# Kernel tuning notes

Hardware: AMD Instinct MI355X
Metric: run time of the kernel (lower is better)

Reference implementation:

```python
import jax, jax.numpy as jnp
import numpy as np

M, N, C = 384, 384, 16
DN = ('NCHW', 'OIHW', 'NCHW')

def _rconv(x, w):
    # real-valued 2D cross-correlation, padding=4 (9x9 kernel, SAME)
    return jax.lax.conv_general_dilated(x, w, (1, 1), ((4, 4), (4, 4)), dimension_numbers=DN)

def _cconv(x, w):
    # complex conv2d decomposed into 4 real convs (matches torch complex conv2d)
    xr, xi, wr, wi = x.real, x.imag, w.real, w.imag
    return (_rconv(xr, wr) - _rconv(xi, wi)) + 1j * (_rconv(xr, wi) + _rconv(xi, wr))

def setup_inputs() -> dict:
    key = jax.random.key(0)
    ks = jax.random.split(key, 8)
    shp = (1, M, N, 2 * C)
    kspace = jax.random.normal(ks[0], shp, jnp.float32)
    row_keep = (jax.random.uniform(ks[1], (M,)) < 0.45).astype(jnp.float32)
    kspace = kspace * row_keep[None, :, None, None]
    z = 0.1 * jax.random.normal(ks[2], shp, jnp.float32)
    prev_kspace = 0.1 * jax.random.normal(ks[3], shp, jnp.float32)
    kernel_r = 0.05 * jax.random.normal(ks[4], (1, 81, C, C), jnp.float32)
    kernel_i = 0.05 * jax.random.normal(ks[5], (1, 81, C, C), jnp.float32)
    miu = jnp.array([0.05], jnp.float32)
    spirit_kernels = jnp.zeros((1,), jnp.float32)  # unused by the module's math
    return {"z": z, "kspace": kspace, "kernel_r": kernel_r, "kernel_i": kernel_i,
            "spirit_kernels": spirit_kernels, "prev_kspace": prev_kspace, "miu": miu}

def _forward(z, kspace, kernel_r, kernel_i, prev_kspace, miu):
    divp = kspace.shape[3] // 2
    kk = kspace[0, :, :, :divp] + 1j * kspace[0, :, :, divp:]  # [m,n,C] complex64
    m, n, no_c = kk.shape
    locs = jnp.abs(kk) > 0                                     # sampling mask
    K = (kernel_r[0] + 1j * kernel_i[0]).reshape(9, 9, no_c, no_c)
    # forward SPIRiT weight: Wf[co,ci,p,q] = K[q,p,ci,co]  (torch permute (3,2,1,0))
    Wf = jnp.transpose(K, (3, 2, 1, 0))
    # adjoint weight: conj, spatial flip, swap in/out channels (exact conv_backward_new)
    Wb = jnp.transpose(jnp.conj(jnp.flip(Wf, (2, 3))), (1, 0, 2, 3))

    def G(x, W):  # [m,n,C] -> [m,n,C] via NCHW complex conv
        y = _cconv(jnp.transpose(x, (2, 0, 1))[None], W)
        return jnp.transpose(y[0], (1, 2, 0))

    mask = lambda x: jnp.where(locs, x, 0)  # selection_operator followed by its adjoint

    def ATA(x):  # x: [1,m,n,C]
        x0 = x[0]
        a2 = mask(x0)                # D^T D x
        b1 = G(x0, Wf) - x0          # (G - I) x
        b2 = G(b1, Wb) - b1          # (G - I)^H (G - I) x
        return (a2 + b2)[None]       # rho = 1

    ws = prev_kspace[:, :, :, :divp] + 1j * prev_kspace[:, :, :, divp:]
    zc = z[:, :, :, :divp] + 1j * z[:, :, :, divp:]
    am = jnp.abs(miu[0])
    DTy = mask(kk)[None]             # D^T D y (y = sampled k-space)
    p = DTy + am * zc - ATA(ws) - am * ws
    r = p
    b = ws

    def step(carry, _):
        b, p, r = carry
        q = ATA(p) + am * p
        rr = jnp.sum(r * jnp.conj(r))
        alpha = rr / jnp.sum(q * jnp.conj(p))
        b_n = b + alpha * p
        r_n = r - alpha * q
        p_n = r_n + (jnp.sum(r_n * jnp.conj(r_n)) / rr) * p
        return (b_n, p_n, r_n), None

    (b, _, _), _ = jax.lax.scan(step, (b, p, r), None, length=10)
    return jnp.concatenate([jnp.real(b), jnp.imag(b)], axis=3)

def reference(z, kspace, kernel_r, kernel_i, spirit_kernels, prev_kspace, miu):
    return _forward(z, kspace, kernel_r, kernel_i, prev_kspace, miu)
```

## Files before the change

### kernel.cpp

```cpp
#include <hip/hip_runtime.h>
#include <stdint.h>


#define MM 384
#define NPIX (MM*MM)
#define N2 (16*NPIX)
#define NRED 512
#define NCBLK 768

typedef __attribute__((ext_vector_type(8))) short short8;
typedef __attribute__((ext_vector_type(4))) float f32x4;
typedef unsigned int u32;

__device__ __forceinline__ float2 block_reduce2(float2 v) {
    #pragma unroll
    for (int off = 32; off > 0; off >>= 1) {
        v.x += __shfl_down(v.x, off);
        v.y += __shfl_down(v.y, off);
    }
    __shared__ float2 tmp[8];
    const int wid = threadIdx.x >> 6, lid = threadIdx.x & 63;
    if (lid == 0) tmp[wid] = v;
    __syncthreads();
    if (threadIdx.x == 0) {
        const int nw = blockDim.x >> 6;
        for (int i = 1; i < nw; ++i) { v.x += tmp[i].x; v.y += tmp[i].y; }
    }
    return v;
}

__device__ __forceinline__ u32 bf16rn(float f) {
    const u32 u = __float_as_uint(f);
    return (u + 0x7FFFu + ((u >> 16) & 1u)) >> 16;
}

__global__ void prep_weights(const float* __restrict__ kr, const float* __restrict__ ki,
                             u32* __restrict__ wbuf) {
    const int e = blockIdx.x * 256 + threadIdx.x;
    if (e >= 20736) return;
    const int lane = e & 63;
    int r = e >> 6;
    const int hf = r & 1; r >>= 1;
    const int q = r % 9; r /= 9;
    const int p = r % 9; r /= 9;
    const int dir = r;
    const int co = lane & 15, g = lane >> 4;
    float vv[8];
    #pragma unroll
    for (int t = 0; t < 8; ++t) {
        const int kc = 8 * g + t;
        const int ci = kc & 15;
        const int isI = kc >> 4;
        int sidx;
        if (dir == 0) sidx = (q*9 + p)*256 + ci*16 + co;
        else          sidx = ((8-q)*9 + (8-p))*256 + co*16 + ci;
        const float wr = kr[sidx];
        const float wi = (dir == 0) ? ki[sidx] : -ki[sidx];
        vv[t] = (hf == 0) ? (isI ? -wi : wr) : (isI ? wr : wi);
    }
    u32 pk[4];
    #pragma unroll
    for (int t = 0; t < 4; ++t) pk[t] = bf16rn(vv[2*t]) | (bf16rn(vv[2*t+1]) << 16);
    u32* o = wbuf + (size_t)(dir*162 + (q*9 + p)*2 + hf)*256 + lane*4;
    *(uint4*)o = make_uint4(pk[0], pk[1], pk[2], pk[3]);
}

__global__ void prep_fields(const float* __restrict__ ks, const float* __restrict__ prev,
                            float2* __restrict__ wsf, uint8_t* __restrict__ mask8) {
    const int pix = blockIdx.x * blockDim.x + threadIdx.x;
    if (pix >= NPIX) return;
    #pragma unroll
    for (int c = 0; c < 16; ++c) {
        const float krr = ks[(size_t)pix*32 + c];
        const float kii = ks[(size_t)pix*32 + c + 16];
        mask8[(size_t)c*NPIX + pix] = (krr != 0.f || kii != 0.f) ? 1 : 0;
        wsf[(size_t)c*NPIX + pix] = make_float2(prev[(size_t)pix*32 + c], prev[(size_t)pix*32 + c + 16]);
    }
}

template<int MODE>
__global__ __launch_bounds__(384, 5)
void conv9(const float2* __restrict__ x, const u32* __restrict__ Wd,
           float2* __restrict__ out, float2* __restrict__ out2,
           const float2* __restrict__ aux, const float* __restrict__ ks,
           const float* __restrict__ z, const uint8_t* __restrict__ mask8,
           const float* __restrict__ miu, float2* __restrict__ partials)
{
    __shared__ __align__(16) char Xs[20*24*64];
    const int t = threadIdx.x;
    const int bi0 = blockIdx.x;
    const int bi = (bi0 & 7) * 96 + (bi0 >> 3);
    const int i0 = (bi / 24) * 12;
    const int j0 = (bi % 24) * 16;
    const int w = t >> 6, lane = t & 63;
    const int hf = (w >= 3) ? 1 : 0;
    const int wr = w - 3*hf;
    const int m = lane & 15, g = lane >> 4;

    for (int u = t; u < 20*24; u += 384) {
        const int col = u % 24, row = u / 24;
        const int row_g = i0 - 4 + row, col_g = j0 - 4 + col;
        const bool valid = ((unsigned)row_g < MM) && ((unsigned)col_g < MM);
        const float2* src = x + (size_t)row_g*MM + col_g;
        float2 v[16];
        #pragma unroll
        for (int ci = 0; ci < 16; ++ci)
            v[ci] = valid ? src[(size_t)ci*NPIX] : make_float2(0.f, 0.f);
        u32 c0[4], c1[4], c2[4], c3[4];
        #pragma unroll
        for (int j = 0; j < 4; ++j) {
            c0[j] = bf16rn(v[2*j].x)     | (bf16rn(v[2*j+1].x) << 16);
            c1[j] = bf16rn(v[8+2*j].x)   | (bf16rn(v[9+2*j].x) << 16);
            c2[j] = bf16rn(v[2*j].y)     | (bf16rn(v[2*j+1].y) << 16);
            c3[j] = bf16rn(v[8+2*j].y)   | (bf16rn(v[9+2*j].y) << 16);
        }
        const int k3 = col & 3;
        char* pb = Xs + (size_t)(row*24 + col)*64;
        *(uint4*)(pb + (((0 ^ k3)) << 4)) = make_uint4(c0[0], c0[1], c0[2], c0[3]);
        *(uint4*)(pb + (((1 ^ k3)) << 4)) = make_uint4(c1[0], c1[1], c1[2], c1[3]);
        *(uint4*)(pb + (((2 ^ k3)) << 4)) = make_uint4(c2[0], c2[1], c2[2], c2[3]);
        *(uint4*)(pb + (((3 ^ k3)) << 4)) = make_uint4(c3[0], c3[1], c3[2], c3[3]);
    }
    __syncthreads();

    f32x4 acc[4];
    #pragma unroll
    for (int a = 0; a < 4; ++a) acc[a] = (f32x4){0.f, 0.f, 0.f, 0.f};

    const char* wl = (const char*)Wd + (lane << 4) + (hf << 10);
    short8 W0, W1, W2, W3, W4, W5, W6, W7, W8;
    short8 X0, X1, X2, X3, X4, X5;

    #define LW(WS, ADDR) do { WS = *(const short8*)(ADDR); } while (0)
    #define MFQ(Xa, Xb, Xc, Xd, WS) do { \
        acc[0] = __builtin_amdgcn_mfma_f32_16x16x32_bf16(WS, Xa, acc[0], 0, 0, 0); \
        acc[1] = __builtin_amdgcn_mfma_f32_16x16x32_bf16(WS, Xb, acc[1], 0, 0, 0); \
        acc[2] = __builtin_amdgcn_mfma_f32_16x16x32_bf16(WS, Xc, acc[2], 0, 0, 0); \
        acc[3] = __builtin_amdgcn_mfma_f32_16x16x32_bf16(WS, Xd, acc[3], 0, 0, 0); } while (0)

    LW(W0, wl);            LW(W1, wl + 2048);   LW(W2, wl + 4096);
    LW(W3, wl + 6144);     LW(W4, wl + 8192);   LW(W5, wl + 10240);
    LW(W6, wl + 12288);    LW(W7, wl + 14336);  LW(W8, wl + 16384);
    {
        const char* xb0 = Xs + (size_t)((4*wr)*24 + m)*64 + ((g ^ (m & 3)) << 4);
        X0 = *(const short8*)(xb0);
        X1 = *(const short8*)(xb0 + 1536);
        X2 = *(const short8*)(xb0 + 2*1536);
        X3 = *(const short8*)(xb0 + 3*1536);
        X4 = *(const short8*)(xb0 + 4*1536);
    }

    #pragma unroll 1
    for (int qq = 0; qq < 9; ++qq) {
        const char* wq = wl + (size_t)qq * 18432 + 18432;
        const int colq = m + qq;
        const char* xb  = Xs + (size_t)((4*wr)*24 + colq)*64 + ((g ^ (colq & 3)) << 4);
        const int colq1 = colq + 1;
        const char* xbn = Xs + (size_t)((4*wr)*24 + colq1)*64 + ((g ^ (colq1 & 3)) << 4);

        MFQ(X0, X1, X2, X3, W0); LW(W0, wq);           X5 = *(const short8*)(xb + 5*1536);
        MFQ(X1, X2, X3, X4, W1); LW(W1, wq + 2048);    X0 = *(const short8*)(xb + 6*1536);
        MFQ(X2, X3, X4, X5, W2); LW(W2, wq + 4096);    X1 = *(const short8*)(xb + 7*1536);
        MFQ(X3, X4, X5, X0, W3); LW(W3, wq + 6144);    X2 = *(const short8*)(xb + 8*1536);
        MFQ(X4, X5, X0, X1, W4); LW(W4, wq + 8192);    X3 = *(const short8*)(xb + 9*1536);
        MFQ(X5, X0, X1, X2, W5); LW(W5, wq + 10240);   X4 = *(const short8*)(xb + 10*1536);
        MFQ(X0, X1, X2, X3, W6); LW(W6, wq + 12288);   X5 = *(const short8*)(xb + 11*1536);
        MFQ(X1, X2, X3, X4, W7); LW(W7, wq + 14336);   X0 = *(const short8*)(xbn);
        MFQ(X2, X3, X4, X5, W8); LW(W8, wq + 16384);   X1 = *(const short8*)(xbn + 1536);
        X2 = *(const short8*)(xbn + 2*1536);
        X3 = *(const short8*)(xbn + 3*1536);
        X4 = *(const short8*)(xbn + 4*1536);
    }
    #undef LW
    #undef MFQ

    __syncthreads();
    {
        char* base = Xs + (size_t)(((hf*12 + 4*wr)*16) + m)*64 + ((g ^ (m & 3)) << 4);
        *(f32x4*)(base)        = acc[0];
        *(f32x4*)(base + 1024) = acc[1];
        *(f32x4*)(base + 2048) = acc[2];
        *(f32x4*)(base + 3072) = acc[3];
    }
    __syncthreads();

    const float am = (MODE >= 1) ? fabsf(miu[0]) : 0.f;
    float2 part = make_float2(0.f, 0.f);
    {
        const int pair = t >> 1, ch = t & 1;
        const int co = pair & 15, row = pair >> 4;
        const int gs = co >> 2, js = co & 3;
        float re[8], im[8];
        #pragma unroll
        for (int k = 0; k < 8; ++k) {
            const int col = ch*8 + k;
            const int off = (row*16 + col)*64 + ((gs ^ (col & 3)) << 4) + js*4;
            re[k] = *(const float*)(Xs + off);
            im[k] = *(const float*)(Xs + off + 12288);
        }
        const int pixb = (i0 + row)*MM + j0 + ch*8;
        const size_t gidx = (size_t)co*NPIX + pixb;
        #pragma unroll
        for (int k = 0; k < 8; ++k) {
            if (MODE == 0) {
                const float2 tc = x[gidx + k];
                out[gidx + k] = make_float2(re[k] - tc.x, im[k] - tc.y);
            } else if (MODE == 1) {
                const float2 tc = x[gidx + k];
                const float2 pc = aux[gidx + k];
                const float mv = mask8[gidx + k] ? 1.f : 0.f;
                const float qr = re[k] - tc.x + (mv + am)*pc.x;
                const float qi = im[k] - tc.y + (mv + am)*pc.y;
                out[gidx + k] = make_float2(qr, qi);
                part.x += qr*pc.x + qi*pc.y;
                part.y += qi*pc.x - qr*pc.y;
            } else {
                const float2 tc = x[gidx + k];
                const float2 wc = aux[gidx + k];
                const float mv = mask8[gidx + k] ? 1.f : 0.f;
                const int pix = pixb + k;
                const float kcr = ks[(size_t)pix*32 + co];
                const float kci = ks[(size_t)pix*32 + co + 16];
                const float zr  = z[(size_t)pix*32 + co];
                const float zi  = z[(size_t)pix*32 + co + 16];
                const float pr = mv*kcr + am*zr - (re[k] - tc.x) - (mv + am)*wc.x;
                const float pi = mv*kci + am*zi - (im[k] - tc.y) - (mv + am)*wc.y;
                out[gidx + k]  = make_float2(pr, pi);
                out2[gidx + k] = make_float2(pr, pi);
                part.x += pr*pr + pi*pi;
            }
        }
    }
    if (MODE >= 1) {
        __syncthreads();
        part = block_reduce2(part);
        if (t == 0) partials[bi] = part;
    }
}

__global__ void finalize_rr(const float2* __restrict__ partials, float* __restrict__ scal, int n) {
    float2 s = make_float2(0.f, 0.f);
    for (int i = threadIdx.x; i < n; i += blockDim.x) { s.x += partials[i].x; s.y += partials[i].y; }
    s = block_reduce2(s);
    if (threadIdx.x == 0) scal[0] = s.x;
}

__global__ void finalize_alpha(const float2* __restrict__ partials, float* __restrict__ scal, int n) {
    float2 s = make_float2(0.f, 0.f);
    for (int i = threadIdx.x; i < n; i += blockDim.x) { s.x += partials[i].x; s.y += partials[i].y; }
    s = block_reduce2(s);
    if (threadIdx.x == 0) {
        const float rr = scal[0];
        const float d = s.x*s.x + s.y*s.y;
        scal[1] =  rr * s.x / d;
        scal[2] = -rr * s.y / d;
    }
}

__global__ void update_r(float2* __restrict__ r, const float2* __restrict__ q,
                         const float* __restrict__ scal, float2* __restrict__ partials) {
    const float ar = scal[1], ai = scal[2];
    float2 s = make_float2(0.f, 0.f);
    for (int e = blockIdx.x*256 + threadIdx.x; e < N2; e += NRED*256) {
        const float2 qv = q[e];
        float2 rv = r[e];
        rv.x -= ar*qv.x - ai*qv.y;
        rv.y -= ar*qv.y + ai*qv.x;
        r[e] = rv;
        s.x += rv.x*rv.x + rv.y*rv.y;
    }
    s = block_reduce2(s);
    if (threadIdx.x == 0) partials[blockIdx.x] = s;
}

__global__ void finalize_beta(const float2* __restrict__ partials, float* __restrict__ scal) {
    float2 v = partials[threadIdx.x];
    v = block_reduce2(v);
    if (threadIdx.x == 0) {
        const float rn = v.x;
        scal[3] = rn / scal[0];
        scal[0] = rn;
    }
}

__global__ void update_pb(float2* __restrict__ p, const float2* __restrict__ r,
                          float2* __restrict__ b, const float* __restrict__ scal) {
    const float ar = scal[1], ai = scal[2], beta = scal[3];
    const int e = blockIdx.x*256 + threadIdx.x;
    if (e < N2) {
        const float2 pv = p[e], rv = r[e];
        float2 bv = b[e];
        bv.x += ar*pv.x - ai*pv.y;
        bv.y += ar*pv.y + ai*pv.x;
        b[e] = bv;
        p[e] = make_float2(rv.x + beta*pv.x, rv.y + beta*pv.y);
    }
}

__global__ void update_bfinal(float2* __restrict__ b, const float2* __restrict__ p,
                              const float* __restrict__ scal) {
    const float ar = scal[1], ai = scal[2];
    const int e = blockIdx.x*256 + threadIdx.x;
    if (e < N2) {
        const float2 pv = p[e];
        float2 bv = b[e];
        bv.x += ar*pv.x - ai*pv.y;
        bv.y += ar*pv.y + ai*pv.x;
        b[e] = bv;
    }
}

__global__ void pack_out(const float2* __restrict__ b, float* __restrict__ out) {
    const int e = blockIdx.x*256 + threadIdx.x;
    if (e >= 32*NPIX) return;
    const int pix = e >> 5;
    const int cc  = e & 31;
    const float2 v = b[(size_t)(cc & 15)*NPIX + pix];
    out[e] = (cc < 16) ? v.x : v.y;
}

extern "C" void kernel_launch(void* const* d_in, const int* in_sizes, int n_in,
                              void* d_out, int out_size, void* d_ws, size_t ws_size,
                              hipStream_t stream) {
    const float* z    = (const float*)d_in[0];
    const float* ks   = (const float*)d_in[1];
    const float* kr   = (const float*)d_in[2];
    const float* ki   = (const float*)d_in[3];
    const float* prev = (const float*)d_in[5];
    const float* miu  = (const float*)d_in[6];
    float* out = (float*)d_out;

    char* w = (char*)d_ws;
    const size_t FB = (size_t)N2 * sizeof(float2);
    float2* wsf = (float2*)w; w += FB;
    float2* pf  = (float2*)w; w += FB;
    float2* rf  = (float2*)w; w += FB;
    float2* qf  = (float2*)w; w += FB;
    float2* tf  = (float2*)w; w += FB;
    u32* wbuf   = (u32*)w;   w += (size_t)2*162*256*sizeof(u32);
    uint8_t* mask8 = (uint8_t*)w; w += (size_t)N2;
    w = (char*)(((uintptr_t)w + 255) & ~(uintptr_t)255);
    float2* partials = (float2*)w; w += (size_t)NCBLK * sizeof(float2);
    float*  scal     = (float*)w;

    const u32* wbF = wbuf;
    const u32* wbB = wbuf + (size_t)162*256;

    prep_weights<<<81, 256, 0, stream>>>(kr, ki, wbuf);
    prep_fields<<<576, 256, 0, stream>>>(ks, prev, wsf, mask8);

    conv9<0><<<NCBLK, 384, 0, stream>>>(wsf, wbF, tf, nullptr, nullptr, nullptr, nullptr, nullptr, nullptr, nullptr);
    conv9<2><<<NCBLK, 384, 0, stream>>>(tf, wbB, pf, rf, wsf, ks, z, mask8, miu, partials);
    finalize_rr<<<1, 256, 0, stream>>>(partials, scal, NCBLK);

    for (int it = 0; it < 10; ++it) {
        conv9<0><<<NCBLK, 384, 0, stream>>>(pf, wbF, tf, nullptr, nullptr, nullptr, nullptr, nullptr, nullptr, nullptr);
        conv9<1><<<NCBLK, 384, 0, stream>>>(tf, wbB, qf, nullptr, pf, nullptr, nullptr, mask8, miu, partials);
        finalize_alpha<<<1, 256, 0, stream>>>(partials, scal, NCBLK);
        if (it < 9) {
            update_r<<<NRED, 256, 0, stream>>>(rf, qf, scal, partials);
            finalize_beta<<<1, NRED, 0, stream>>>(partials, scal);
            update_pb<<<9216, 256, 0, stream>>>(pf, rf, wsf, scal);
        } else {
            update_bfinal<<<9216, 256, 0, stream>>>(wsf, pf, scal);
        }
    }

    pack_out<<<18432, 256, 0, stream>>>(wsf, out);
}
```

Baseline: 1.046 ms.

## Stagger per-wave tap start and widen LDS register window in MFMA conv loop

Each wave now begins the 9-column tap loop at an offset given by its wave index, cycling modulo 9, so different waves read different weight rows and LDS columns at the same moment. The rolling X register window grows from 6 to 12 short8 registers, so the next column's rows are prefetched during the current column's MFMAs. The intent is to reduce L2/LDS contention and hide LDS latency behind the MFMAs. The cost is higher VGPR pressure, which may lower occupancy, plus extra modulo index arithmetic inside the loop.

```diff
diff --git a/kernel.cpp b/kernel.cpp
--- a/kernel.cpp
+++ b/kernel.cpp
@@ -128,8 +128,9 @@
     for (int a = 0; a < 4; ++a) acc[a] = (f32x4){0.f, 0.f, 0.f, 0.f};
 
     const char* wl = (const char*)Wd + (lane << 4) + (hf << 10);
+    const int q_off = w;
     short8 W0, W1, W2, W3, W4, W5, W6, W7, W8;
-    short8 X0, X1, X2, X3, X4, X5;
+    short8 XR0, XR1, XR2, XR3, XR4, XR5, XR6, XR7, XR8, XR9, XR10, XR11;
 
     #define LW(WS, ADDR) do { WS = *(const short8*)(ADDR); } while (0)
     #define MFQ(Xa, Xb, Xc, Xd, WS) do { \
@@ -138,38 +139,43 @@
         acc[2] = __builtin_amdgcn_mfma_f32_16x16x32_bf16(WS, Xc, acc[2], 0, 0, 0); \
         acc[3] = __builtin_amdgcn_mfma_f32_16x16x32_bf16(WS, Xd, acc[3], 0, 0, 0); } while (0)
 
-    LW(W0, wl);            LW(W1, wl + 2048);   LW(W2, wl + 4096);
-    LW(W3, wl + 6144);     LW(W4, wl + 8192);   LW(W5, wl + 10240);
-    LW(W6, wl + 12288);    LW(W7, wl + 14336);  LW(W8, wl + 16384);
     {
-        const char* xb0 = Xs + (size_t)((4*wr)*24 + m)*64 + ((g ^ (m & 3)) << 4);
-        X0 = *(const short8*)(xb0);
-        X1 = *(const short8*)(xb0 + 1536);
-        X2 = *(const short8*)(xb0 + 2*1536);
-        X3 = *(const short8*)(xb0 + 3*1536);
-        X4 = *(const short8*)(xb0 + 4*1536);
+        const char* wq0 = wl + (size_t)q_off * 18432;
+        LW(W0, wq0);           LW(W1, wq0 + 2048);   LW(W2, wq0 + 4096);
+        LW(W3, wq0 + 6144);    LW(W4, wq0 + 8192);   LW(W5, wq0 + 10240);
+        LW(W6, wq0 + 12288);   LW(W7, wq0 + 14336);  LW(W8, wq0 + 16384);
+        const int xcol0 = m + q_off;
+        const char* xb0 = Xs + (size_t)((4*wr)*24 + xcol0)*64 + ((g ^ (xcol0 & 3)) << 4);
+        XR0 = *(const short8*)(xb0);
+        XR1 = *(const short8*)(xb0 + 1536);
+        XR2 = *(const short8*)(xb0 + 2*1536);
+        XR3 = *(const short8*)(xb0 + 3*1536);
+        XR4 = *(const short8*)(xb0 + 4*1536);
+        XR5 = *(const short8*)(xb0 + 5*1536);
+        XR6 = *(const short8*)(xb0 + 6*1536);
+        XR7 = *(const short8*)(xb0 + 7*1536);
+        XR8 = *(const short8*)(xb0 + 8*1536);
     }
 
     #pragma unroll 1
     for (int qq = 0; qq < 9; ++qq) {
-        const char* wq = wl + (size_t)qq * 18432 + 18432;
-        const int colq = m + qq;
-        const char* xb  = Xs + (size_t)((4*wr)*24 + colq)*64 + ((g ^ (colq & 3)) << 4);
-        const int colq1 = colq + 1;
-        const char* xbn = Xs + (size_t)((4*wr)*24 + colq1)*64 + ((g ^ (colq1 & 3)) << 4);
-
-        MFQ(X0, X1, X2, X3, W0); LW(W0, wq);           X5 = *(const short8*)(xb + 5*1536);
-        MFQ(X1, X2, X3, X4, W1); LW(W1, wq + 2048);    X0 = *(const short8*)(xb + 6*1536);
-        MFQ(X2, X3, X4, X5, W2); LW(W2, wq + 4096);    X1 = *(const short8*)(xb + 7*1536);
-        MFQ(X3, X4, X5, X0, W3); LW(W3, wq + 6144);    X2 = *(const short8*)(xb + 8*1536);
-        MFQ(X4, X5, X0, X1, W4); LW(W4, wq + 8192);    X3 = *(const short8*)(xb + 9*1536);
-        MFQ(X5, X0, X1, X2, W5); LW(W5, wq + 10240);   X4 = *(const short8*)(xb + 10*1536);
-        MFQ(X0, X1, X2, X3, W6); LW(W6, wq + 12288);   X5 = *(const short8*)(xb + 11*1536);
-        MFQ(X1, X2, X3, X4, W7); LW(W7, wq + 14336);   X0 = *(const short8*)(xbn);
-        MFQ(X2, X3, X4, X5, W8); LW(W8, wq + 16384);   X1 = *(const short8*)(xbn + 1536);
-        X2 = *(const short8*)(xbn + 2*1536);
-        X3 = *(const short8*)(xbn + 3*1536);
-        X4 = *(const short8*)(xbn + 4*1536);
+        int cq = q_off + qq;  if (cq >= 9) cq -= 9;
+        int cqn = cq + 1;     if (cqn >= 9) cqn -= 9;
+        const char* wq = wl + (size_t)cqn * 18432;
+        const int xcol  = m + cq;
+        const int xcoln = m + cqn;
+        const char* xb  = Xs + (size_t)((4*wr)*24 + xcol )*64 + ((g ^ (xcol  & 3)) << 4);
+        const char* xbn = Xs + (size_t)((4*wr)*24 + xcoln)*64 + ((g ^ (xcoln & 3)) << 4);
+
+        MFQ(XR0, XR1, XR2, XR3, W0); LW(W0, wq);           XR9  = *(const short8*)(xb + 9*1536);  XR0 = *(const short8*)(xbn);
+        MFQ(XR1, XR2, XR3, XR4, W1); LW(W1, wq + 2048);    XR10 = *(const short8*)(xb + 10*1536); XR1 = *(const short8*)(xbn + 1536);
+        MFQ(XR2, XR3, XR4, XR5, W2); LW(W2, wq + 4096);    XR11 = *(const short8*)(xb + 11*1536); XR2 = *(const short8*)(xbn + 2*1536);
+        MFQ(XR3, XR4, XR5, XR6, W3); LW(W3, wq + 6144);    XR3 = *(const short8*)(xbn + 3*1536);
+        MFQ(XR4, XR5, XR6, XR7, W4); LW(W4, wq + 8192);    XR4 = *(const short8*)(xbn + 4*1536);
+        MFQ(XR5, XR6, XR7, XR8, W5); LW(W5, wq + 10240);   XR5 = *(const short8*)(xbn + 5*1536);
+        MFQ(XR6, XR7, XR8, XR9, W6); LW(W6, wq + 12288);   XR6 = *(const short8*)(xbn + 6*1536);
+        MFQ(XR7, XR8, XR9, XR10, W7); LW(W7, wq + 14336);  XR7 = *(const short8*)(xbn + 7*1536);
+        MFQ(XR8, XR9, XR10, XR11, W8); LW(W8, wq + 16384); XR8 = *(const short8*)(xbn + 8*1536);
     }
     #undef LW
     #undef MFQ
```

New measurement: 1.066 ms. About the same (+1.9%).

## Stage per-column conv weights in shared memory instead of register-prefetching from global

Applied to the files above, without the earlier changes.

Each block now copies the 18 KB weight slice for a kernel column into LDS cooperatively, with a barrier before and after, then reads weights from LDS inside the MFMA loop. Before, each wave loaded its weights straight from global into nine registers, prefetching the next column. This aims to cut redundant global and L2 weight traffic and register pressure. In exchange it adds two block barriers per column, 18 KB more LDS per block (which may lower occupancy), and drops the cross-iteration prefetch that hid latency.

```diff
diff --git a/kernel.cpp b/kernel.cpp
--- a/kernel.cpp
+++ b/kernel.cpp
@@ -87,6 +87,7 @@
            const float* __restrict__ miu, float2* __restrict__ partials)
 {
     __shared__ __align__(16) char Xs[20*24*64];
+    __shared__ __align__(16) char Wsh[9*2048];
     const int t = threadIdx.x;
     const int bi0 = blockIdx.x;
     const int bi = (bi0 & 7) * 96 + (bi0 >> 3);
@@ -127,51 +128,44 @@
     #pragma unroll
     for (int a = 0; a < 4; ++a) acc[a] = (f32x4){0.f, 0.f, 0.f, 0.f};
 
-    const char* wl = (const char*)Wd + (lane << 4) + (hf << 10);
-    short8 W0, W1, W2, W3, W4, W5, W6, W7, W8;
-    short8 X0, X1, X2, X3, X4, X5;
-
-    #define LW(WS, ADDR) do { WS = *(const short8*)(ADDR); } while (0)
+    const char* WdC = (const char*)Wd;
+    const char* wls = Wsh + (hf << 10) + (lane << 4);
+
     #define MFQ(Xa, Xb, Xc, Xd, WS) do { \
         acc[0] = __builtin_amdgcn_mfma_f32_16x16x32_bf16(WS, Xa, acc[0], 0, 0, 0); \
         acc[1] = __builtin_amdgcn_mfma_f32_16x16x32_bf16(WS, Xb, acc[1], 0, 0, 0); \
         acc[2] = __builtin_amdgcn_mfma_f32_16x16x32_bf16(WS, Xc, acc[2], 0, 0, 0); \
         acc[3] = __builtin_amdgcn_mfma_f32_16x16x32_bf16(WS, Xd, acc[3], 0, 0, 0); } while (0)
 
-    LW(W0, wl);            LW(W1, wl + 2048);   LW(W2, wl + 4096);
-    LW(W3, wl + 6144);     LW(W4, wl + 8192);   LW(W5, wl + 10240);
-    LW(W6, wl + 12288);    LW(W7, wl + 14336);  LW(W8, wl + 16384);
-    {
-        const char* xb0 = Xs + (size_t)((4*wr)*24 + m)*64 + ((g ^ (m & 3)) << 4);
-        X0 = *(const short8*)(xb0);
-        X1 = *(const short8*)(xb0 + 1536);
-        X2 = *(const short8*)(xb0 + 2*1536);
-        X3 = *(const short8*)(xb0 + 3*1536);
-        X4 = *(const short8*)(xb0 + 4*1536);
-    }
-
     #pragma unroll 1
     for (int qq = 0; qq < 9; ++qq) {
-        const char* wq = wl + (size_t)qq * 18432 + 18432;
+        if (qq) __syncthreads();
+        {
+            const uint4* wsrc = (const uint4*)(WdC + (size_t)qq * 18432);
+            uint4* wdst = (uint4*)Wsh;
+            wdst[t]       = wsrc[t];
+            wdst[t + 384] = wsrc[t + 384];
+            wdst[t + 768] = wsrc[t + 768];
+        }
+        __syncthreads();
+
         const int colq = m + qq;
-        const char* xb  = Xs + (size_t)((4*wr)*24 + colq)*64 + ((g ^ (colq & 3)) << 4);
-        const int colq1 = colq + 1;
-        const char* xbn = Xs + (size_t)((4*wr)*24 + colq1)*64 + ((g ^ (colq1 & 3)) << 4);
-
-        MFQ(X0, X1, X2, X3, W0); LW(W0, wq);           X5 = *(const short8*)(xb + 5*1536);
-        MFQ(X1, X2, X3, X4, W1); LW(W1, wq + 2048);    X0 = *(const short8*)(xb + 6*1536);
-        MFQ(X2, X3, X4, X5, W2); LW(W2, wq + 4096);    X1 = *(const short8*)(xb + 7*1536);
-        MFQ(X3, X4, X5, X0, W3); LW(W3, wq + 6144);    X2 = *(const short8*)(xb + 8*1536);
-        MFQ(X4, X5, X0, X1, W4); LW(W4, wq + 8192);    X3 = *(const short8*)(xb + 9*1536);
-        MFQ(X5, X0, X1, X2, W5); LW(W5, wq + 10240);   X4 = *(const short8*)(xb + 10*1536);
-        MFQ(X0, X1, X2, X3, W6); LW(W6, wq + 12288);   X5 = *(const short8*)(xb + 11*1536);
-        MFQ(X1, X2, X3, X4, W7); LW(W7, wq + 14336);   X0 = *(const short8*)(xbn);
-        MFQ(X2, X3, X4, X5, W8); LW(W8, wq + 16384);   X1 = *(const short8*)(xbn + 1536);
-        X2 = *(const short8*)(xbn + 2*1536);
-        X3 = *(const short8*)(xbn + 3*1536);
-        X4 = *(const short8*)(xbn + 4*1536);
-    }
-    #undef LW
+        const char* xb = Xs + (size_t)((4*wr)*24 + colq)*64 + ((g ^ (colq & 3)) << 4);
+        short8 X0 = *(const short8*)(xb);
+        short8 X1 = *(const short8*)(xb + 1536);
+        short8 X2 = *(const short8*)(xb + 2*1536);
+        short8 X3 = *(const short8*)(xb + 3*1536);
+        short8 X4, WT;
+        WT = *(const short8*)(wls);          X4 = *(const short8*)(xb + 4*1536);  MFQ(X0, X1, X2, X3, WT);
+        WT = *(const short8*)(wls + 2048);   X0 = *(const short8*)(xb + 5*1536);  MFQ(X1, X2, X3, X4, WT);
+        WT = *(const short8*)(wls + 4096);   X1 = *(const short8*)(xb + 6*1536);  MFQ(X2, X3, X4, X0, WT);
+        WT = *(const short8*)(wls + 6144);   X2 = *(const short8*)(xb + 7*1536);  MFQ(X3, X4, X0, X1, WT);
+        WT = *(const short8*)(wls + 8192);   X3 = *(const short8*)(xb + 8*1536);  MFQ(X4, X0, X1, X2, WT);
+        WT = *(const short8*)(wls + 10240);  X4 = *(const short8*)(xb + 9*1536);  MFQ(X0, X1, X2, X3, WT);
+        WT = *(const short8*)(wls + 12288);  X0 = *(const short8*)(xb + 10*1536); MFQ(X1, X2, X3, X4, WT);
+        WT = *(const short8*)(wls + 14336);  X1 = *(const short8*)(xb + 11*1536); MFQ(X2, X3, X4, X0, WT);
+        WT = *(const short8*)(wls + 16384);                                       MFQ(X3, X4, X0, X1, WT);
+    }
     #undef MFQ
 
     __syncthreads();
```

Result: slower. 1.175 ms (+12.3%).
